# Kernel optimization log

Hardware: AMD Instinct MI355X
Metric: run time of the kernel (lower is better)

## Reference

```python
import jax, jax.numpy as jnp
import numpy as np

NUM_MAPS = 512
NUM_BLOCKS = 2
ZG = 512
HID = min(96, NUM_MAPS)          # shared query / attention hidden dim
SEQ = 8                           # hardcoded inner sequence length
H1 = min(NUM_MAPS // 32, 3)       # num_heads1 = 3
H2 = NUM_MAPS // 32               # num_heads2 = 16
NPROC = NUM_BLOCKS * 4            # 4 FiLM param types per block


def _mha(q, k, v, nheads):
    """Multi-head attention. q:(Lq,D) k,v:(Lk,D) -> (Lq,D)."""
    Lq, D = q.shape
    Lk = k.shape[0]
    d = D // nheads
    qh = q.reshape(Lq, nheads, d).transpose(1, 0, 2)   # (h,Lq,d)
    kh = k.reshape(Lk, nheads, d).transpose(1, 0, 2)
    vh = v.reshape(Lk, nheads, d).transpose(1, 0, 2)
    A = jax.nn.softmax(jnp.einsum('hqd,hkd->hqk', qh, kh) / jnp.sqrt(jnp.asarray(D, q.dtype)))
    O = jnp.einsum('hqk,hkd->hqd', A, vh)
    return O.transpose(1, 0, 2).reshape(Lq, D)


def setup_inputs() -> dict:
    key = jax.random.key(0)
    ks = jax.random.split(key, 20)
    s = 0.05
    n = jax.random.normal
    return {
        'gate': jax.random.uniform(ks[0], (1, SEQ), dtype=jnp.float32),
        'x': n(ks[1], (1, ZG), dtype=jnp.float32),
        # shared_layer_alphaC : Linear(ZG, NUM_MAPS) + Sigmoid
        'Wa': n(ks[2], (ZG, NUM_MAPS)) * s, 'ba': jnp.zeros((NUM_MAPS,)),
        # shared_layer_Query : Linear(ZG, HID) + ReLU
        'Wqr': n(ks[3], (ZG, HID)) * s, 'bqr': jnp.zeros((HID,)),
        # stacked FiLM params: [block, {g1,b1,g2,b2}, num_maps, 8]
        'P': n(ks[4], (NUM_BLOCKS, 4, NUM_MAPS, SEQ)) * 0.2,
        'De': n(ks[5], (NUM_BLOCKS, 4, NUM_MAPS, SEQ)) * 0.01,
        'regs': n(ks[6], (NUM_BLOCKS, 4, NUM_MAPS)) * 0.001,
        # SMAB_small processor weights, stacked over the 8 processors
        'Wq1': n(ks[7], (NPROC, NUM_MAPS, HID)) * s,
        'Wk1': n(ks[8], (NPROC, NUM_MAPS, HID)) * s,
        'Wv1': n(ks[9], (NPROC, NUM_MAPS, HID)) * s,
        'fc1': n(ks[10], (NPROC, HID, HID)) * s,
        'Wq2': n(ks[11], (NPROC, HID, HID)) * s,
        'Wk2': n(ks[12], (NPROC, HID, HID)) * s,
        'Wv2': n(ks[13], (NPROC, HID, HID)) * s,
        'fc2': n(ks[14], (NPROC, HID, HID)) * s,
        'Wo': n(ks[15], (NPROC, HID, NUM_MAPS)) * s,
    }


def reference(gate, x, Wa, ba, Wqr, bqr, P, De, regs,
              Wq1, Wk1, Wv1, fc1, Wq2, Wk2, Wv2, fc2, Wo):
    alpha = jax.nn.sigmoid(x @ Wa + ba).reshape(-1)        # (NUM_MAPS,)
    q = jax.nn.relu(x @ Wqr + bqr)                          # (1, HID)

    # per-processor key/value set: transpose(1,0).view(1,8,num_maps)
    K_all = P.reshape(NPROC, NUM_MAPS, SEQ).transpose(0, 2, 1)  # (8procs, 8, NUM_MAPS)

    def smab(K, wq1, wk1, wv1, f1, wq2, wk2, wv2, f2, wo):
        # stage 1: self-attention over the 8-element set (num_heads1)
        Qk = K @ wq1                                        # (8, HID)
        H = Qk + _mha(Qk, K @ wk1, K @ wv1, H1)
        H = H + jax.nn.relu(H @ f1)
        # stage 2: task query attends to the set (num_heads2)
        Qq = q @ wq2                                        # (1, HID)
        O = Qq + _mha(Qq, H @ wk2, H @ wv2, H2)
        O = O + jax.nn.relu(O @ f2)
        return (O @ wo)[0]                                  # (NUM_MAPS,)

    trans = jax.vmap(smab)(K_all, Wq1, Wk1, Wv1, fc1, Wq2, Wk2, Wv2, fc2, Wo)
    trans = trans.reshape(NUM_BLOCKS, 4, NUM_MAPS)

    de = (De * gate[0]).sum(-1)                             # (NB,4,NUM_MAPS)
    mix = alpha * trans + (1.0 - alpha) * de
    offs = jnp.array([1.0, 0.0, 1.0, 0.0], dtype=mix.dtype).reshape(1, 4, 1)
    # gamma gets +1 offset, beta does not
    return mix * regs + offs
```

## Files before the change

kernel.cpp:

```cpp
#include <hip/hip_runtime.h>
#include <hip/hip_bf16.h>
#include <math.h>


#define WS_ALPHA 0
#define WS_Q     512
#define WS_QKV   608
#define WS_K2    19040
#define WS_V2    25184
#define WS_QQ    31328

__global__ __launch_bounds__(256) void kA_qkv_alpha_q(
    const float* __restrict__ x, const float* __restrict__ Wa,
    const float* __restrict__ ba, const float* __restrict__ Wqr,
    const float* __restrict__ bqr, const float* __restrict__ P,
    const float* __restrict__ Wq1, const float* __restrict__ Wk1,
    const float* __restrict__ Wv1, float* __restrict__ ws)
{
    __shared__ float sK[8 * 528];
    __shared__ float sp[2048];
    const int blk = blockIdx.x, tid = threadIdx.x;

    if (blk < 144) {
        const int proc = blk & 7, rem = blk >> 3;
        const int mat = rem / 6, six = rem % 6;
        const int hl = tid & 15, ks = tid >> 4;
        const int h = six * 16 + hl;
        const float* W = (mat == 0 ? Wq1 : (mat == 1 ? Wk1 : Wv1))
                         + proc * 49152 + (ks * 32) * 96 + h;
        float wreg[32];
        #pragma unroll
        for (int m2 = 0; m2 < 32; ++m2) wreg[m2] = W[m2 * 96];
        const float4* P4 = (const float4*)(P + proc * 4096);
        for (int i = tid; i < 1024; i += 256) {
            float4 v = P4[i];
            const int c = i >> 1, off = (i & 1) * 4;
            const int cp = c + (c >> 5);
            sK[(off + 0) * 528 + cp] = v.x;
            sK[(off + 1) * 528 + cp] = v.y;
            sK[(off + 2) * 528 + cp] = v.z;
            sK[(off + 3) * 528 + cp] = v.w;
        }
        __syncthreads();
        const float* Kb = sK + ks * 33;
        float acc[8] = {0.f,0.f,0.f,0.f,0.f,0.f,0.f,0.f};
        #pragma unroll
        for (int m2 = 0; m2 < 32; ++m2) {
            const float w = wreg[m2];
            const float* Kc = Kb + m2;
            #pragma unroll
            for (int s = 0; s < 8; ++s) acc[s] += Kc[s * 528] * w;
        }
        float* spb = sp + ks * 128 + hl * 8;
        #pragma unroll
        for (int s = 0; s < 8; ++s) spb[s] = acc[s];
        __syncthreads();
        if (tid < 128) {
            float a = 0.f;
            #pragma unroll
            for (int u = 0; u < 16; ++u) a += sp[u * 128 + tid];
            const int hl2 = tid >> 3, s = tid & 7;
            ws[WS_QKV + proc * 2304 + mat * 768 + s * 96 + six * 16 + hl2] = a;
        }
    } else if (blk < 176) {
        const int ml = tid & 15, ks = tid >> 4;
        const int m = (blk - 144) * 16 + ml;
        const float* W = Wa + (ks * 32) * 512 + m;
        float wreg[32];
        #pragma unroll
        for (int k = 0; k < 32; ++k) wreg[k] = W[k * 512];
        for (int k = tid; k < 512; k += 256) sK[k] = x[k];
        __syncthreads();
        const float* xq = sK + ks * 32;
        float acc = 0.f;
        #pragma unroll
        for (int k = 0; k < 32; ++k) acc += xq[k] * wreg[k];
        sp[tid] = acc;
        __syncthreads();
        if (tid < 16) {
            float a = ba[(blk - 144) * 16 + tid];
            #pragma unroll
            for (int u = 0; u < 16; ++u) a += sp[u * 16 + tid];
            ws[WS_ALPHA + (blk - 144) * 16 + tid] = 1.f / (1.f + __expf(-a));
        }
    } else {
        const int hl = tid & 15, ks = tid >> 4;
        const int h = (blk - 176) * 16 + hl;
        const float* W = Wqr + (ks * 32) * 96 + h;
        float wreg[32];
        #pragma unroll
        for (int k = 0; k < 32; ++k) wreg[k] = W[k * 96];
        for (int k = tid; k < 512; k += 256) sK[k] = x[k];
        __syncthreads();
        const float* xq = sK + ks * 32;
        float acc = 0.f;
        #pragma unroll
        for (int k = 0; k < 32; ++k) acc += xq[k] * wreg[k];
        sp[tid] = acc;
        __syncthreads();
        if (tid < 16) {
            float a = bqr[(blk - 176) * 16 + tid];
            #pragma unroll
            for (int u = 0; u < 16; ++u) a += sp[u * 16 + tid];
            ws[WS_Q + (blk - 176) * 16 + tid] = fmaxf(a, 0.f);
        }
    }
}

__global__ __launch_bounds__(256) void kB_attn1_fc1_kv2(
    const float* __restrict__ fc1w, const float* __restrict__ Wk2,
    const float* __restrict__ Wv2, const float* __restrict__ Wq2,
    float* __restrict__ ws)
{
    const int b = blockIdx.x, tid = threadIdx.x;
    const float rs = 0.10206207261596577f;

    if (b < 48) {
        const int proc = b & 7, slot = b >> 3;
        const int mat = slot / 3, t = slot % 3;
        __shared__ float sQk[768], sKk[768], sVv[768], sH[768], sH2[768], sS[192];
        __shared__ float sWf1[9216];
        __shared__ float sWkv[96 * 32];

        {
            const float4* F4 = (const float4*)fc1w + proc * 2304;
            float4* D4 = (float4*)sWf1;
            #pragma unroll
            for (int r = 0; r < 9; ++r) D4[tid + 256 * r] = F4[tid + 256 * r];
            const float4* KV4 = (const float4*)(mat ? Wv2 : Wk2);
            float4* E4 = (float4*)sWkv;
            #pragma unroll
            for (int r = 0; r < 3; ++r) {
                const int idx = tid + 256 * r;
                const int row = idx >> 3, q4 = idx & 7;
                E4[row * 8 + q4] = KV4[proc * 2304 + row * 24 + t * 8 + q4];
            }
        }
        const float* qkv = ws + WS_QKV + proc * 2304;
        for (int i = tid; i < 768; i += 256) {
            sQk[i] = qkv[i]; sKk[i] = qkv[768 + i]; sVv[i] = qkv[1536 + i];
        }
        __syncthreads();

        if (tid < 192) {
            const int h0 = tid / 64, r64 = tid % 64, si = r64 / 8, sk = r64 % 8;
            float acc = 0.f;
            #pragma unroll
            for (int d = 0; d < 32; ++d)
                acc += sQk[si * 96 + h0 * 32 + d] * sKk[sk * 96 + h0 * 32 + d];
            sS[tid] = acc * rs;
        }
        __syncthreads();
        if (tid < 24) {
            float* row = sS + tid * 8;
            float mx = row[0];
            #pragma unroll
            for (int k = 1; k < 8; ++k) mx = fmaxf(mx, row[k]);
            float e[8], sum = 0.f;
            #pragma unroll
            for (int k = 0; k < 8; ++k) { e[k] = __expf(row[k] - mx); sum += e[k]; }
            const float inv = 1.f / sum;
            #pragma unroll
            for (int k = 0; k < 8; ++k) row[k] = e[k] * inv;
        }
        __syncthreads();
        if (tid < 192) {
            const int h0 = tid / 64, r64 = tid % 64, si = r64 / 8, dq = r64 % 8;
            const float* e = sS + h0 * 64 + si * 8;
            float o0 = 0.f, o1 = 0.f, o2 = 0.f, o3 = 0.f;
            #pragma unroll
            for (int k = 0; k < 8; ++k) {
                const float ek = e[k];
                const float* v = sVv + k * 96 + h0 * 32 + dq * 4;
                o0 += ek*v[0]; o1 += ek*v[1]; o2 += ek*v[2]; o3 += ek*v[3];
            }
            const int base = si * 96 + h0 * 32 + dq * 4;
            sH[base+0] = sQk[base+0] + o0;  sH[base+1] = sQk[base+1] + o1;
            sH[base+2] = sQk[base+2] + o2;  sH[base+3] = sQk[base+3] + o3;
        }
        __syncthreads();
        #pragma unroll
        for (int r = 0; r < 3; ++r) {
            const int idx = tid + 256 * r, s = idx / 96, j = idx % 96;
            const float* Hs = sH + s * 96;
            float acc = 0.f;
            #pragma unroll
            for (int i = 0; i < 96; ++i) acc += Hs[i] * sWf1[i * 96 + j];
            sH2[idx] = sH[idx] + fmaxf(acc, 0.f);
        }
        __syncthreads();
        const int s = tid >> 5, jl = tid & 31, j = t * 32 + jl;
        const float* Hs = sH2 + s * 96;
        float acc = 0.f;
        #pragma unroll
        for (int i = 0; i < 96; ++i) acc += Hs[i] * sWkv[i * 32 + jl];
        ws[(mat ? WS_V2 : WS_K2) + proc * 768 + s * 96 + j] = acc;
    } else {
        const int b2 = b - 48, proc = b2 & 7, t = b2 >> 3;
        __shared__ float sq[96], sp[256];
        if (tid < 96) sq[tid] = ws[WS_Q + tid];
        __syncthreads();
        const int jl = tid & 31, ks = tid >> 5;
        const int j = 32 * t + jl;
        const float* W = Wq2 + proc * 9216 + j;
        float acc = 0.f;
        #pragma unroll
        for (int i = 0; i < 12; ++i)
            acc += sq[12 * ks + i] * W[(12 * ks + i) * 96];
        sp[tid] = acc;
        __syncthreads();
        if (ks == 0) {
            float a = 0.f;
            #pragma unroll
            for (int u = 0; u < 8; ++u) a += sp[jl + 32 * u];
            ws[WS_QQ + proc * 96 + j] = a;
        }
    }
}

__global__ __launch_bounds__(256) void kC_attn2_fc2_out(
    const float* __restrict__ gate, const float* __restrict__ De,
    const float* __restrict__ regs, const float* __restrict__ fc2w,
    const float* __restrict__ Wo, const float* __restrict__ ws,
    float* __restrict__ out)
{
    const int b = blockIdx.x, proc = b & 7, e = b >> 3, tid = threadIdx.x;
    __shared__ float sK2[768], sV2[768];
    __shared__ float sQq[96], sO[96], sOf[96], sE2[128], sg[8], sp[256];
    __shared__ float sWf2[9216];
    __shared__ float sWo[96 * 64];
    const float rs = 0.10206207261596577f;

    {
        const float4* F4 = (const float4*)fc2w + proc * 2304;
        float4* D4 = (float4*)sWf2;
        #pragma unroll
        for (int r = 0; r < 9; ++r) D4[tid + 256 * r] = F4[tid + 256 * r];
        const float4* W4 = (const float4*)Wo;
        float4* E4 = (float4*)sWo;
        #pragma unroll
        for (int r = 0; r < 6; ++r) {
            const int idx = tid + 256 * r;
            const int row = idx >> 4, q4 = idx & 15;
            E4[row * 16 + q4] = W4[proc * 12288 + row * 128 + e * 16 + q4];
        }
    }
    const int ml = tid & 63, ks = tid >> 6;
    const int m = 64 * e + ml;
    const float4* Dp4 = (const float4*)(De + proc * 4096 + m * 8);
    const float4 d0 = Dp4[0], d1 = Dp4[1];
    const float av = ws[WS_ALPHA + m];
    const float rg = regs[proc * 512 + m];
    for (int i = tid; i < 768; i += 256) {
        sK2[i] = ws[WS_K2 + proc * 768 + i];
        sV2[i] = ws[WS_V2 + proc * 768 + i];
    }
    if (tid < 96) sQq[tid] = ws[WS_QQ + proc * 96 + tid];
    else if (tid >= 96 && tid < 104) sg[tid - 96] = gate[tid - 96];
    __syncthreads();

    if (tid < 16) {
        const int h0 = tid;
        float lg[8], mx = -1e30f;
        #pragma unroll
        for (int k = 0; k < 8; ++k) {
            float acc = 0.f;
            #pragma unroll
            for (int d = 0; d < 6; ++d)
                acc += sQq[h0 * 6 + d] * sK2[k * 96 + h0 * 6 + d];
            lg[k] = acc * rs; mx = fmaxf(mx, lg[k]);
        }
        float ex[8], sum = 0.f;
        #pragma unroll
        for (int k = 0; k < 8; ++k) { ex[k] = __expf(lg[k] - mx); sum += ex[k]; }
        const float inv = 1.f / sum;
        #pragma unroll
        for (int k = 0; k < 8; ++k) sE2[h0 * 8 + k] = ex[k] * inv;
    }
    __syncthreads();
    if (tid < 96) {
        const int h0 = tid / 6;
        float o = 0.f;
        #pragma unroll
        for (int k = 0; k < 8; ++k) o += sE2[h0 * 8 + k] * sV2[k * 96 + tid];
        sO[tid] = sQq[tid] + o;
    }
    __syncthreads();
    if (tid < 192) {
        const int j = tid % 96, k2 = tid / 96;
        const float* Os = sO + k2 * 48;
        float acc = 0.f;
        #pragma unroll
        for (int i = 0; i < 48; ++i) acc += Os[i] * sWf2[(k2 * 48 + i) * 96 + j];
        sp[tid] = acc;
    }
    __syncthreads();
    if (tid < 96) sOf[tid] = sO[tid] + fmaxf(sp[tid] + sp[96 + tid], 0.f);
    __syncthreads();

    float acc = 0.f;
    #pragma unroll
    for (int i = 0; i < 24; ++i)
        acc += sOf[24 * ks + i] * sWo[(24 * ks + i) * 64 + ml];
    sp[tid] = acc;
    __syncthreads();
    if (ks == 0) {
        const float tr = sp[ml] + sp[ml + 64] + sp[ml + 128] + sp[ml + 192];
        const float de = d0.x * sg[0] + d0.y * sg[1] + d0.z * sg[2] + d0.w * sg[3]
                       + d1.x * sg[4] + d1.y * sg[5] + d1.z * sg[6] + d1.w * sg[7];
        const float mix = av * tr + (1.f - av) * de;
        const int pt = proc & 3;
        const float off = (pt == 0 || pt == 2) ? 1.f : 0.f;
        out[proc * 512 + m] = mix * rg + off;
    }
}

extern "C" void kernel_launch(void* const* d_in, const int* in_sizes, int n_in,
                              void* d_out, int out_size, void* d_ws, size_t ws_size,
                              hipStream_t stream)
{
    const float* gate = (const float*)d_in[0];
    const float* x    = (const float*)d_in[1];
    const float* Wa   = (const float*)d_in[2];
    const float* ba   = (const float*)d_in[3];
    const float* Wqr  = (const float*)d_in[4];
    const float* bqr  = (const float*)d_in[5];
    const float* P    = (const float*)d_in[6];
    const float* De   = (const float*)d_in[7];
    const float* regs = (const float*)d_in[8];
    const float* Wq1  = (const float*)d_in[9];
    const float* Wk1  = (const float*)d_in[10];
    const float* Wv1  = (const float*)d_in[11];
    const float* fc1  = (const float*)d_in[12];
    const float* Wq2  = (const float*)d_in[13];
    const float* Wk2  = (const float*)d_in[14];
    const float* Wv2  = (const float*)d_in[15];
    const float* fc2  = (const float*)d_in[16];
    const float* Wo   = (const float*)d_in[17];
    float* ws = (float*)d_ws;

    hipLaunchKernelGGL(kA_qkv_alpha_q, dim3(182), dim3(256), 0, stream,
                       x, Wa, ba, Wqr, bqr, P, Wq1, Wk1, Wv1, ws);
    hipLaunchKernelGGL(kB_attn1_fc1_kv2, dim3(72), dim3(256), 0, stream,
                       fc1, Wk2, Wv2, Wq2, ws);
    hipLaunchKernelGGL(kC_attn2_fc2_out, dim3(64), dim3(256), 0, stream,
                       gate, De, regs, fc2, Wo, ws, (float*)d_out);
}
```

Measured before the change: 107.6 us.

## Fuse attention-1, FC1, KV2 and output stages into one kernel with redundant compute

Merges the second and third kernels into a single 64-block kernel. Each block now recomputes the full stage-1 attention, fc1, Q2, K2 and V2 projections for its processor, which removes one launch and the workspace round trip. The fc2 and Wo weights are read straight from global memory instead of being staged in LDS. In exchange, every block does 8x redundant work and loads about 136KB into LDS, which lowers occupancy and lengthens the serial chain inside each block.

After: 115.4 us. 1.07x slower.

```diff
diff --git a/kernel.cpp b/kernel.cpp
--- a/kernel.cpp
+++ b/kernel.cpp
@@ -6,9 +6,26 @@
 #define WS_ALPHA 0
 #define WS_Q     512
 #define WS_QKV   608
-#define WS_K2    19040
-#define WS_V2    25184
-#define WS_QQ    31328
+
+#define SQK 0
+#define SKK 768
+#define SVV 1536
+#define SH  2304
+#define SH2 3072
+#define SK2 3840
+#define SV2 4608
+#define SQ  5376
+#define SQQ 5472
+#define SO  5568
+#define SOF 5664
+#define SE2 5760
+#define SG  5888
+#define SS  5896
+#define SP  6088
+#define WF1 6344
+#define WK2 15560
+#define WV2 24776
+#define LDS_FLOATS 33992
 
 __global__ __launch_bounds__(256) void kA_qkv_alpha_q(
     const float* __restrict__ x, const float* __restrict__ Wa,
@@ -107,158 +124,113 @@
     }
 }
 
-__global__ __launch_bounds__(256) void kB_attn1_fc1_kv2(
-    const float* __restrict__ fc1w, const float* __restrict__ Wk2,
-    const float* __restrict__ Wv2, const float* __restrict__ Wq2,
-    float* __restrict__ ws)
-{
-    const int b = blockIdx.x, tid = threadIdx.x;
-    const float rs = 0.10206207261596577f;
-
-    if (b < 48) {
-        const int proc = b & 7, slot = b >> 3;
-        const int mat = slot / 3, t = slot % 3;
-        __shared__ float sQk[768], sKk[768], sVv[768], sH[768], sH2[768], sS[192];
-        __shared__ float sWf1[9216];
-        __shared__ float sWkv[96 * 32];
-
-        {
-            const float4* F4 = (const float4*)fc1w + proc * 2304;
-            float4* D4 = (float4*)sWf1;
-            #pragma unroll
-            for (int r = 0; r < 9; ++r) D4[tid + 256 * r] = F4[tid + 256 * r];
-            const float4* KV4 = (const float4*)(mat ? Wv2 : Wk2);
-            float4* E4 = (float4*)sWkv;
-            #pragma unroll
-            for (int r = 0; r < 3; ++r) {
-                const int idx = tid + 256 * r;
-                const int row = idx >> 3, q4 = idx & 7;
-                E4[row * 8 + q4] = KV4[proc * 2304 + row * 24 + t * 8 + q4];
-            }
-        }
-        const float* qkv = ws + WS_QKV + proc * 2304;
-        for (int i = tid; i < 768; i += 256) {
-            sQk[i] = qkv[i]; sKk[i] = qkv[768 + i]; sVv[i] = qkv[1536 + i];
-        }
-        __syncthreads();
-
-        if (tid < 192) {
-            const int h0 = tid / 64, r64 = tid % 64, si = r64 / 8, sk = r64 % 8;
-            float acc = 0.f;
-            #pragma unroll
-            for (int d = 0; d < 32; ++d)
-                acc += sQk[si * 96 + h0 * 32 + d] * sKk[sk * 96 + h0 * 32 + d];
-            sS[tid] = acc * rs;
-        }
-        __syncthreads();
-        if (tid < 24) {
-            float* row = sS + tid * 8;
-            float mx = row[0];
-            #pragma unroll
-            for (int k = 1; k < 8; ++k) mx = fmaxf(mx, row[k]);
-            float e[8], sum = 0.f;
-            #pragma unroll
-            for (int k = 0; k < 8; ++k) { e[k] = __expf(row[k] - mx); sum += e[k]; }
-            const float inv = 1.f / sum;
-            #pragma unroll
-            for (int k = 0; k < 8; ++k) row[k] = e[k] * inv;
-        }
-        __syncthreads();
-        if (tid < 192) {
-            const int h0 = tid / 64, r64 = tid % 64, si = r64 / 8, dq = r64 % 8;
-            const float* e = sS + h0 * 64 + si * 8;
-            float o0 = 0.f, o1 = 0.f, o2 = 0.f, o3 = 0.f;
-            #pragma unroll
-            for (int k = 0; k < 8; ++k) {
-                const float ek = e[k];
-                const float* v = sVv + k * 96 + h0 * 32 + dq * 4;
-                o0 += ek*v[0]; o1 += ek*v[1]; o2 += ek*v[2]; o3 += ek*v[3];
-            }
-            const int base = si * 96 + h0 * 32 + dq * 4;
-            sH[base+0] = sQk[base+0] + o0;  sH[base+1] = sQk[base+1] + o1;
-            sH[base+2] = sQk[base+2] + o2;  sH[base+3] = sQk[base+3] + o3;
-        }
-        __syncthreads();
-        #pragma unroll
-        for (int r = 0; r < 3; ++r) {
-            const int idx = tid + 256 * r, s = idx / 96, j = idx % 96;
-            const float* Hs = sH + s * 96;
-            float acc = 0.f;
-            #pragma unroll
-            for (int i = 0; i < 96; ++i) acc += Hs[i] * sWf1[i * 96 + j];
-            sH2[idx] = sH[idx] + fmaxf(acc, 0.f);
-        }
-        __syncthreads();
-        const int s = tid >> 5, jl = tid & 31, j = t * 32 + jl;
-        const float* Hs = sH2 + s * 96;
-        float acc = 0.f;
-        #pragma unroll
-        for (int i = 0; i < 96; ++i) acc += Hs[i] * sWkv[i * 32 + jl];
-        ws[(mat ? WS_V2 : WS_K2) + proc * 768 + s * 96 + j] = acc;
-    } else {
-        const int b2 = b - 48, proc = b2 & 7, t = b2 >> 3;
-        __shared__ float sq[96], sp[256];
-        if (tid < 96) sq[tid] = ws[WS_Q + tid];
-        __syncthreads();
-        const int jl = tid & 31, ks = tid >> 5;
-        const int j = 32 * t + jl;
-        const float* W = Wq2 + proc * 9216 + j;
-        float acc = 0.f;
-        #pragma unroll
-        for (int i = 0; i < 12; ++i)
-            acc += sq[12 * ks + i] * W[(12 * ks + i) * 96];
-        sp[tid] = acc;
-        __syncthreads();
-        if (ks == 0) {
-            float a = 0.f;
-            #pragma unroll
-            for (int u = 0; u < 8; ++u) a += sp[jl + 32 * u];
-            ws[WS_QQ + proc * 96 + j] = a;
-        }
-    }
-}
-
-__global__ __launch_bounds__(256) void kC_attn2_fc2_out(
+__global__ __launch_bounds__(256) void kBC_all(
     const float* __restrict__ gate, const float* __restrict__ De,
-    const float* __restrict__ regs, const float* __restrict__ fc2w,
-    const float* __restrict__ Wo, const float* __restrict__ ws,
+    const float* __restrict__ regs, const float* __restrict__ fc1w,
+    const float* __restrict__ Wq2,  const float* __restrict__ Wk2,
+    const float* __restrict__ Wv2,  const float* __restrict__ fc2w,
+    const float* __restrict__ Wo,   const float* __restrict__ ws,
     float* __restrict__ out)
 {
+    extern __shared__ float sm[];
     const int b = blockIdx.x, proc = b & 7, e = b >> 3, tid = threadIdx.x;
-    __shared__ float sK2[768], sV2[768];
-    __shared__ float sQq[96], sO[96], sOf[96], sE2[128], sg[8], sp[256];
-    __shared__ float sWf2[9216];
-    __shared__ float sWo[96 * 64];
     const float rs = 0.10206207261596577f;
 
     {
-        const float4* F4 = (const float4*)fc2w + proc * 2304;
-        float4* D4 = (float4*)sWf2;
-        #pragma unroll
-        for (int r = 0; r < 9; ++r) D4[tid + 256 * r] = F4[tid + 256 * r];
-        const float4* W4 = (const float4*)Wo;
-        float4* E4 = (float4*)sWo;
-        #pragma unroll
-        for (int r = 0; r < 6; ++r) {
-            const int idx = tid + 256 * r;
-            const int row = idx >> 4, q4 = idx & 15;
-            E4[row * 16 + q4] = W4[proc * 12288 + row * 128 + e * 16 + q4];
-        }
-    }
+        const float4* F1 = (const float4*)fc1w + proc * 2304;
+        const float4* K4 = (const float4*)Wk2 + proc * 2304;
+        const float4* V4 = (const float4*)Wv2 + proc * 2304;
+        float4* d1 = (float4*)(sm + WF1);
+        float4* d2 = (float4*)(sm + WK2);
+        float4* d3 = (float4*)(sm + WV2);
+        #pragma unroll
+        for (int r = 0; r < 9; ++r) {
+            const int i = tid + 256 * r;
+            d1[i] = F1[i]; d2[i] = K4[i]; d3[i] = V4[i];
+        }
+    }
+    const float* qkv = ws + WS_QKV + proc * 2304;
+    for (int i = tid; i < 768; i += 256) {
+        sm[SQK + i] = qkv[i];
+        sm[SKK + i] = qkv[768 + i];
+        sm[SVV + i] = qkv[1536 + i];
+    }
+    if (tid < 96) sm[SQ + tid] = ws[WS_Q + tid];
+    else if (tid < 104) sm[SG + tid - 96] = gate[tid - 96];
     const int ml = tid & 63, ks = tid >> 6;
     const int m = 64 * e + ml;
     const float4* Dp4 = (const float4*)(De + proc * 4096 + m * 8);
-    const float4 d0 = Dp4[0], d1 = Dp4[1];
+    const float4 d0 = Dp4[0], d1v = Dp4[1];
     const float av = ws[WS_ALPHA + m];
     const float rg = regs[proc * 512 + m];
-    for (int i = tid; i < 768; i += 256) {
-        sK2[i] = ws[WS_K2 + proc * 768 + i];
-        sV2[i] = ws[WS_V2 + proc * 768 + i];
-    }
-    if (tid < 96) sQq[tid] = ws[WS_QQ + proc * 96 + tid];
-    else if (tid >= 96 && tid < 104) sg[tid - 96] = gate[tid - 96];
-    __syncthreads();
-
+    __syncthreads();
+
+    if (tid < 192) {
+        const int h0 = tid / 64, r64 = tid % 64, si = r64 / 8, sk = r64 % 8;
+        float acc = 0.f;
+        #pragma unroll
+        for (int d = 0; d < 32; ++d)
+            acc += sm[SQK + si * 96 + h0 * 32 + d] * sm[SKK + sk * 96 + h0 * 32 + d];
+        sm[SS + tid] = acc * rs;
+    }
+    __syncthreads();
+    if (tid < 24) {
+        float* row = sm + SS + tid * 8;
+        float mx = row[0];
+        #pragma unroll
+        for (int k = 1; k < 8; ++k) mx = fmaxf(mx, row[k]);
+        float ex[8], sum = 0.f;
+        #pragma unroll
+        for (int k = 0; k < 8; ++k) { ex[k] = __expf(row[k] - mx); sum += ex[k]; }
+        const float inv = 1.f / sum;
+        #pragma unroll
+        for (int k = 0; k < 8; ++k) row[k] = ex[k] * inv;
+    }
+    __syncthreads();
+    if (tid < 192) {
+        const int h0 = tid / 64, r64 = tid % 64, si = r64 / 8, dq = r64 % 8;
+        const float* ep = sm + SS + h0 * 64 + si * 8;
+        float o0 = 0.f, o1 = 0.f, o2 = 0.f, o3 = 0.f;
+        #pragma unroll
+        for (int k = 0; k < 8; ++k) {
+            const float ek = ep[k];
+            const float* v = sm + SVV + k * 96 + h0 * 32 + dq * 4;
+            o0 += ek*v[0]; o1 += ek*v[1]; o2 += ek*v[2]; o3 += ek*v[3];
+        }
+        const int base = si * 96 + h0 * 32 + dq * 4;
+        sm[SH+base+0] = sm[SQK+base+0] + o0;  sm[SH+base+1] = sm[SQK+base+1] + o1;
+        sm[SH+base+2] = sm[SQK+base+2] + o2;  sm[SH+base+3] = sm[SQK+base+3] + o3;
+    }
+    __syncthreads();
+    #pragma unroll
+    for (int r = 0; r < 3; ++r) {
+        const int idx = tid + 256 * r, s = idx / 96, j = idx % 96;
+        const float* Hs = sm + SH + s * 96;
+        float acc = 0.f;
+        #pragma unroll
+        for (int i = 0; i < 96; ++i) acc += Hs[i] * sm[WF1 + i * 96 + j];
+        sm[SH2 + idx] = sm[SH + idx] + fmaxf(acc, 0.f);
+    }
+    if (tid < 96) {
+        const float* W = Wq2 + proc * 9216 + tid;
+        float acc = 0.f;
+        #pragma unroll
+        for (int i = 0; i < 96; ++i) acc += sm[SQ + i] * W[i * 96];
+        sm[SQQ + tid] = acc;
+    }
+    __syncthreads();
+    #pragma unroll
+    for (int r = 0; r < 6; ++r) {
+        const int idx = tid + 256 * r;
+        const int mat = idx / 768, rr = idx % 768, s = rr / 96, j = rr % 96;
+        const float* Hs = sm + SH2 + s * 96;
+        const float* Wt = sm + (mat ? WV2 : WK2) + j;
+        float acc = 0.f;
+        #pragma unroll
+        for (int i = 0; i < 96; ++i) acc += Hs[i] * Wt[i * 96];
+        sm[(mat ? SV2 : SK2) + rr] = acc;
+    }
+    __syncthreads();
     if (tid < 16) {
         const int h0 = tid;
         float lg[8], mx = -1e30f;
@@ -267,7 +239,7 @@
             float acc = 0.f;
             #pragma unroll
             for (int d = 0; d < 6; ++d)
-                acc += sQq[h0 * 6 + d] * sK2[k * 96 + h0 * 6 + d];
+                acc += sm[SQQ + h0 * 6 + d] * sm[SK2 + k * 96 + h0 * 6 + d];
             lg[k] = acc * rs; mx = fmaxf(mx, lg[k]);
         }
         float ex[8], sum = 0.f;
@@ -275,39 +247,42 @@
         for (int k = 0; k < 8; ++k) { ex[k] = __expf(lg[k] - mx); sum += ex[k]; }
         const float inv = 1.f / sum;
         #pragma unroll
-        for (int k = 0; k < 8; ++k) sE2[h0 * 8 + k] = ex[k] * inv;
+        for (int k = 0; k < 8; ++k) sm[SE2 + h0 * 8 + k] = ex[k] * inv;
     }
     __syncthreads();
     if (tid < 96) {
         const int h0 = tid / 6;
         float o = 0.f;
         #pragma unroll
-        for (int k = 0; k < 8; ++k) o += sE2[h0 * 8 + k] * sV2[k * 96 + tid];
-        sO[tid] = sQq[tid] + o;
-    }
-    __syncthreads();
-    if (tid < 192) {
-        const int j = tid % 96, k2 = tid / 96;
-        const float* Os = sO + k2 * 48;
-        float acc = 0.f;
-        #pragma unroll
-        for (int i = 0; i < 48; ++i) acc += Os[i] * sWf2[(k2 * 48 + i) * 96 + j];
-        sp[tid] = acc;
-    }
-    __syncthreads();
-    if (tid < 96) sOf[tid] = sO[tid] + fmaxf(sp[tid] + sp[96 + tid], 0.f);
-    __syncthreads();
-
-    float acc = 0.f;
-    #pragma unroll
-    for (int i = 0; i < 24; ++i)
-        acc += sOf[24 * ks + i] * sWo[(24 * ks + i) * 64 + ml];
-    sp[tid] = acc;
+        for (int k = 0; k < 8; ++k)
+            o += sm[SE2 + h0 * 8 + k] * sm[SV2 + k * 96 + tid];
+        sm[SO + tid] = sm[SQQ + tid] + o;
+    }
+    __syncthreads();
+    if (tid < 96) {
+        const float* W = fc2w + proc * 9216 + tid;
+        float acc = 0.f;
+        #pragma unroll
+        for (int i = 0; i < 96; ++i) acc += sm[SO + i] * W[i * 96];
+        sm[SOF + tid] = sm[SO + tid] + fmaxf(acc, 0.f);
+    }
+    __syncthreads();
+    {
+        const float* W = Wo + proc * 49152 + m;
+        float acc = 0.f;
+        #pragma unroll
+        for (int i = 0; i < 24; ++i)
+            acc += sm[SOF + 24 * ks + i] * W[(24 * ks + i) * 512];
+        sm[SP + tid] = acc;
+    }
     __syncthreads();
     if (ks == 0) {
-        const float tr = sp[ml] + sp[ml + 64] + sp[ml + 128] + sp[ml + 192];
-        const float de = d0.x * sg[0] + d0.y * sg[1] + d0.z * sg[2] + d0.w * sg[3]
-                       + d1.x * sg[4] + d1.y * sg[5] + d1.z * sg[6] + d1.w * sg[7];
+        const float tr = sm[SP + ml] + sm[SP + ml + 64]
+                       + sm[SP + ml + 128] + sm[SP + ml + 192];
+        const float de = d0.x * sm[SG+0] + d0.y * sm[SG+1]
+                       + d0.z * sm[SG+2] + d0.w * sm[SG+3]
+                       + d1v.x * sm[SG+4] + d1v.y * sm[SG+5]
+                       + d1v.z * sm[SG+6] + d1v.w * sm[SG+7];
         const float mix = av * tr + (1.f - av) * de;
         const int pt = proc & 3;
         const float off = (pt == 0 || pt == 2) ? 1.f : 0.f;
@@ -341,8 +316,8 @@
 
     hipLaunchKernelGGL(kA_qkv_alpha_q, dim3(182), dim3(256), 0, stream,
                        x, Wa, ba, Wqr, bqr, P, Wq1, Wk1, Wv1, ws);
-    hipLaunchKernelGGL(kB_attn1_fc1_kv2, dim3(72), dim3(256), 0, stream,
-                       fc1, Wk2, Wv2, Wq2, ws);
-    hipLaunchKernelGGL(kC_attn2_fc2_out, dim3(64), dim3(256), 0, stream,
-                       gate, De, regs, fc2, Wo, ws, (float*)d_out);
+    hipLaunchKernelGGL(kBC_all, dim3(64), dim3(256),
+                       LDS_FLOATS * sizeof(float), stream,
+                       gate, De, regs, fc1, Wq2, Wk2, Wv2, fc2, Wo,
+                       ws, (float*)d_out);
 }
```
